# Kernel optimization log

Measured on AMD Instinct MI355X. Metric: run time of the kernel, lower is better.

Reference implementation:

```python
import jax, jax.numpy as jnp
import numpy as np

B, S, E = 2, 2048, 2048
H, G = 16, 4
HD = E // H          # 128
GD = HD * G          # 512
NGH = H // G         # 4 (tile factor for K/V heads)


def setup_inputs() -> dict:
    key = jax.random.key(0)
    ks = jax.random.split(key, 6)
    sc = 0.02
    return {
        "x": jax.random.normal(ks[0], (B, S, E), dtype=jnp.float32),
        "mask": jnp.ones((B, S, S), dtype=jnp.int32),
        "Wq": jax.random.normal(ks[1], (E, E), dtype=jnp.float32) * sc,
        "bq": jnp.zeros((E,), dtype=jnp.float32),
        "Wk": jax.random.normal(ks[2], (E, GD), dtype=jnp.float32) * sc,
        "bk": jnp.zeros((GD,), dtype=jnp.float32),
        "Wv": jax.random.normal(ks[3], (E, GD), dtype=jnp.float32) * sc,
        "bv": jnp.zeros((GD,), dtype=jnp.float32),
        "Wo": jax.random.normal(ks[4], (E, E), dtype=jnp.float32) * sc,
        "bo": jnp.zeros((E,), dtype=jnp.float32),
    }


def reference(x, mask, Wq, bq, Wk, bk, Wv, bv, Wo, bo):
    b, s, _ = x.shape
    # projections
    q = x @ Wq + bq                                   # [B,S,E]
    k = x @ Wk + bk                                   # [B,S,GD]
    v = x @ Wv + bv                                   # [B,S,GD]
    q = q.reshape(b, s, H, HD).transpose(0, 2, 1, 3)  # [B,H,S,hd]
    k = k.reshape(b, s, G, HD).transpose(0, 2, 1, 3)  # [B,G,S,hd]
    v = v.reshape(b, s, G, HD).transpose(0, 2, 1, 3)
    # torch .repeat(1, NGH, 1, 1): tile groups -> head h uses group h % G
    k = jnp.tile(k, (1, NGH, 1, 1))                   # [B,H,S,hd]
    v = jnp.tile(v, (1, NGH, 1, 1))
    scale = 1.0 / np.sqrt(HD).astype(np.float32)
    scores = jnp.einsum("bhqd,bhkd->bhqk", q, k) * scale
    m = mask[:, None, :, :]                           # [B,1,S,S]
    scores = jnp.where(m == 0, jnp.float32(-10000.0), scores)
    attn = jax.nn.softmax(scores, axis=-1)
    out = jnp.einsum("bhqk,bhkd->bhqd", attn, v)      # [B,H,S,hd]
    out = out.transpose(0, 2, 1, 3).reshape(b, s, E)  # [B,S,E]
    return out @ Wo + bo
```

## Files before the change

kernel.cpp:

```cpp
#include <hip/hip_runtime.h>

#define B_ 2
#define S_ 2048
#define E_ 2048
#define H_ 16
#define G_ 4
#define HD_ 128
#define GD_ 512
#define KVLD_ 1024
#define QKVN_ 3072
#define M_ (B_*S_)

using u16 = unsigned short;
using u32 = unsigned int;
typedef __attribute__((ext_vector_type(8))) short short8;
typedef __attribute__((ext_vector_type(4))) float f32x4;

#define QSCL 0.12751891114f
#define MASKED_L2 (-14427.0f)

__device__ __forceinline__ u16 f2bf(float f) {
  union { float f; unsigned u; } v; v.f = f;
  unsigned r = v.u + 0x7fff + ((v.u >> 16) & 1);
  return (u16)(r >> 16);
}

__device__ __forceinline__ void async16(const void* g, void* l) {
  __builtin_amdgcn_global_load_lds((const __attribute__((address_space(1))) unsigned int*)g,
                                   (__attribute__((address_space(3))) unsigned int*)l, 16, 0, 0);
}

__global__ __launch_bounds__(256) void cast_plus(const float* __restrict__ in,
                                                 u16* __restrict__ out, int n4,
                                                 const float* __restrict__ ba,
                                                 const float* __restrict__ bbk,
                                                 const float* __restrict__ bc,
                                                 float* __restrict__ bo) {
  if ((int)blockIdx.x >= (n4 + 255) / 256) {
    int t = (blockIdx.x - (n4 + 255) / 256) * 256 + threadIdx.x;
    if (t < 2048) bo[t] = ba[t];
    else if (t < 2560) bo[t] = bbk[t - 2048];
    else if (t < 3072) bo[t] = bc[t - 2560];
    return;
  }
  int i = blockIdx.x * 256 + threadIdx.x;
  if (i >= n4) return;
  float4 v = ((const float4*)in)[i];
  union { u16 o[4]; uint2 u; } pk;
  pk.o[0] = f2bf(v.x); pk.o[1] = f2bf(v.y); pk.o[2] = f2bf(v.z); pk.o[3] = f2bf(v.w);
  *(uint2*)(out + (size_t)i * 4) = pk.u;
}

__global__ __launch_bounds__(256) void transpose_cast4(const float* __restrict__ Wq,
                                                       const float* __restrict__ Wk,
                                                       const float* __restrict__ Wv,
                                                       const float* __restrict__ Wo,
                                                       u16* __restrict__ Wqkvt,
                                                       u16* __restrict__ Wot) {
  __shared__ u16 tile[64 * 72];
  int b = blockIdx.x;
  const float* W; u16* Wt; int N, bx;
  if (b < 1024)      { W = Wq; Wt = Wqkvt;                     N = E_;  bx = b;        }
  else if (b < 1280) { W = Wk; Wt = Wqkvt + (size_t)2048 * E_; N = GD_; bx = b - 1024; }
  else if (b < 1536) { W = Wv; Wt = Wqkvt + (size_t)2560 * E_; N = GD_; bx = b - 1280; }
  else               { W = Wo; Wt = Wot;                       N = E_;  bx = b - 1536; }
  int nbx = N / 64;
  int n0 = (bx % nbx) * 64, k0 = (bx / nbx) * 64;
  int t = threadIdx.x;
  int row = t >> 2;
  int seg = t & 3;
  const float* src = W + (size_t)(k0 + row) * N + n0 + seg * 16;
  #pragma unroll
  for (int i = 0; i < 4; ++i) {
    float4 v = *(const float4*)(src + i * 4);
    int nl = seg * 16 + i * 4;
    tile[(nl + 0) * 72 + row] = f2bf(v.x);
    tile[(nl + 1) * 72 + row] = f2bf(v.y);
    tile[(nl + 2) * 72 + row] = f2bf(v.z);
    tile[(nl + 3) * 72 + row] = f2bf(v.w);
  }
  __syncthreads();
  int nl = t >> 2, s2 = t & 3;
  u16* dst = Wt + (size_t)(n0 + nl) * E_ + k0 + s2 * 16;
  *(uint4*)dst       = *(const uint4*)&tile[nl * 72 + s2 * 16];
  *(uint4*)(dst + 8) = *(const uint4*)&tile[nl * 72 + s2 * 16 + 8];
}

__global__ __launch_bounds__(256) void transpose_v(const u16* __restrict__ KVb, u16* __restrict__ Vtg) {
  __shared__ u16 tile[64 * 72];
  int kv0 = blockIdx.x * 64;
  int gn0 = blockIdx.y * 64;
  int t = threadIdx.x;
  int row = t >> 2, seg = t & 3;
  int prow = (row & 15) * 4 + (row >> 4);
  const u16* src = KVb + (size_t)(kv0 + row) * KVLD_ + 512 + gn0 + seg * 16;
  union { uint4 v; u16 s[8]; } a, b;
  a.v = *(const uint4*)src; b.v = *(const uint4*)(src + 8);
  #pragma unroll
  for (int j = 0; j < 8; ++j) tile[(seg * 16 + j) * 72 + prow] = a.s[j];
  #pragma unroll
  for (int j = 0; j < 8; ++j) tile[(seg * 16 + 8 + j) * 72 + prow] = b.s[j];
  __syncthreads();
  int gl = t >> 2, ks2 = t & 3;
  int bb = kv0 >> 11;
  int s0 = kv0 & 2047;
  int gn = gn0 + gl;
  u16* dst = Vtg + (size_t)(bb * 512 + gn) * S_ + s0 + ks2 * 16;
  *(uint4*)dst       = *(const uint4*)&tile[gl * 72 + ks2 * 16];
  *(uint4*)(dst + 8) = *(const uint4*)&tile[gl * 72 + ks2 * 16 + 8];
}

__global__ __launch_bounds__(256) void mask_flags(const int* __restrict__ mask, int* __restrict__ flags) {
  int idx = blockIdx.x * 4 + (threadIdx.x >> 6);
  int lane = threadIdx.x & 63;
  int bb = idx >> 12, rg = (idx >> 5) & 127, kt = idx & 31;
  const int* base = mask + ((size_t)bb * S_ + rg * 16) * S_ + kt * 64;
  int row = lane >> 2, c0 = (lane & 3) * 16;
  int ok = 1;
  #pragma unroll
  for (int i = 0; i < 4; ++i) {
    int4 v = *(const int4*)&base[(size_t)row * S_ + c0 + i * 4];
    ok &= (v.x != 0) & (v.y != 0) & (v.z != 0) & (v.w != 0);
  }
  ok = __all(ok) ? 1 : 0;
  if (lane == 0) flags[idx] = ok;
}

__global__ __launch_bounds__(256) void gemm_qkv(const u16* __restrict__ A, const u16* __restrict__ Bt,
                                                const float* __restrict__ bias,
                                                u16* __restrict__ Qb, u16* __restrict__ KVb, int K) {
  __shared__ u16 As[2][128 * 32];
  __shared__ u16 Bs[2][128 * 32];
  int nbx = gridDim.x;
  int bid = blockIdx.y * nbx + blockIdx.x;
  int chunk = (nbx * gridDim.y) >> 3;
  int swz = (bid & 7) * chunk + (bid >> 3);
  int n0 = (swz % nbx) * 128, m0 = (swz / nbx) * 128;
  int t = threadIdx.x;
  int w = t >> 6, lane = t & 63, c = lane & 15, q = lane >> 4;
  int wm = w & 1, wn = w >> 1;
  int r0 = t >> 2;
  int kcs = ((t & 3) ^ ((t >> 3) & 3)) * 8;
  const u16* Ag0 = A  + (size_t)(m0 + r0) * K + kcs;
  const u16* Ag1 = A  + (size_t)(m0 + 64 + r0) * K + kcs;
  const u16* Bg0 = Bt + (size_t)(n0 + r0) * K + kcs;
  const u16* Bg1 = Bt + (size_t)(n0 + 64 + r0) * K + kcs;
  int roff = (q ^ ((c >> 1) & 3)) * 8;
  f32x4 acc[4][4] = {};
  async16(Ag0, &As[0][t * 8]);
  async16(Ag1, &As[0][2048 + t * 8]);
  async16(Bg0, &Bs[0][t * 8]);
  async16(Bg1, &Bs[0][2048 + t * 8]);
  for (int k0 = 0; k0 < K; k0 += 32) {
    int cur = (k0 >> 5) & 1;
    __syncthreads();
    if (k0 + 32 < K) {
      async16(Ag0 + k0 + 32, &As[cur ^ 1][t * 8]);
      async16(Ag1 + k0 + 32, &As[cur ^ 1][2048 + t * 8]);
      async16(Bg0 + k0 + 32, &Bs[cur ^ 1][t * 8]);
      async16(Bg1 + k0 + 32, &Bs[cur ^ 1][2048 + t * 8]);
    }
    short8 af[4], bf[4];
    #pragma unroll
    for (int i = 0; i < 4; ++i) {
      af[i] = *(const short8*)&As[cur][(wm * 64 + i * 16 + c) * 32 + roff];
      bf[i] = *(const short8*)&Bs[cur][(wn * 64 + i * 16 + c) * 32 + roff];
    }
    #pragma unroll
    for (int i = 0; i < 4; ++i)
      #pragma unroll
      for (int j = 0; j < 4; ++j)
        acc[i][j] = __builtin_amdgcn_mfma_f32_16x16x32_bf16(af[i], bf[j], acc[i][j], 0, 0, 0);
  }
  int isq = (n0 < 2048);
  #pragma unroll
  for (int i = 0; i < 4; ++i) {
    int mrow_base = m0 + wm * 64 + i * 16 + q * 4;
    #pragma unroll
    for (int j = 0; j < 4; ++j) {
      int coln = n0 + wn * 64 + j * 16 + c;
      float bv = bias[coln];
      #pragma unroll
      for (int r = 0; r < 4; ++r) {
        float v = acc[i][j][r] + bv;
        if (isq) Qb[(size_t)(mrow_base + r) * E_ + coln] = f2bf(v * QSCL);
        else     KVb[(size_t)(mrow_base + r) * KVLD_ + coln - 2048] = f2bf(v);
      }
    }
  }
}

__global__ __launch_bounds__(256) void gemm_k(const u16* __restrict__ A, const u16* __restrict__ Bt,
                                              const float* __restrict__ bias, float* __restrict__ Cout,
                                              int M, int N, int K) {
  __shared__ u16 As[2][128 * 32];
  __shared__ u16 Bs[2][128 * 32];
  int nbx = gridDim.x;
  int bid = blockIdx.y * nbx + blockIdx.x;
  int chunk = (nbx * gridDim.y) >> 3;
  int swz = (bid & 7) * chunk + (bid >> 3);
  int n0 = (swz % nbx) * 128, m0 = (swz / nbx) * 128;
  int t = threadIdx.x;
  int w = t >> 6, lane = t & 63, c = lane & 15, q = lane >> 4;
  int wm = w & 1, wn = w >> 1;
  int r0 = t >> 2;
  int kcs = ((t & 3) ^ ((t >> 3) & 3)) * 8;
  const u16* Ag0 = A  + (size_t)(m0 + r0) * K + kcs;
  const u16* Ag1 = A  + (size_t)(m0 + 64 + r0) * K + kcs;
  const u16* Bg0 = Bt + (size_t)(n0 + r0) * K + kcs;
  const u16* Bg1 = Bt + (size_t)(n0 + 64 + r0) * K + kcs;
  int roff = (q ^ ((c >> 1) & 3)) * 8;
  f32x4 acc[4][4] = {};
  async16(Ag0, &As[0][t * 8]);
  async16(Ag1, &As[0][2048 + t * 8]);
  async16(Bg0, &Bs[0][t * 8]);
  async16(Bg1, &Bs[0][2048 + t * 8]);
  for (int k0 = 0; k0 < K; k0 += 32) {
    int cur = (k0 >> 5) & 1;
    __syncthreads();
    if (k0 + 32 < K) {
      async16(Ag0 + k0 + 32, &As[cur ^ 1][t * 8]);
      async16(Ag1 + k0 + 32, &As[cur ^ 1][2048 + t * 8]);
      async16(Bg0 + k0 + 32, &Bs[cur ^ 1][t * 8]);
      async16(Bg1 + k0 + 32, &Bs[cur ^ 1][2048 + t * 8]);
    }
    short8 af[4], bf[4];
    #pragma unroll
    for (int i = 0; i < 4; ++i) {
      af[i] = *(const short8*)&As[cur][(wm * 64 + i * 16 + c) * 32 + roff];
      bf[i] = *(const short8*)&Bs[cur][(wn * 64 + i * 16 + c) * 32 + roff];
    }
    #pragma unroll
    for (int i = 0; i < 4; ++i)
      #pragma unroll
      for (int j = 0; j < 4; ++j)
        acc[i][j] = __builtin_amdgcn_mfma_f32_16x16x32_bf16(af[i], bf[j], acc[i][j], 0, 0, 0);
  }
  #pragma unroll
  for (int i = 0; i < 4; ++i) {
    int mrow_base = m0 + wm * 64 + i * 16 + q * 4;
    #pragma unroll
    for (int j = 0; j < 4; ++j) {
      int coln = n0 + wn * 64 + j * 16 + c;
      float bv = bias[coln];
      #pragma unroll
      for (int r = 0; r < 4; ++r)
        Cout[(size_t)(mrow_base + r) * N + coln] = acc[i][j][r] + bv;
    }
  }
}

__global__ __launch_bounds__(512) void attn_k(const u16* __restrict__ Q, const u16* __restrict__ KVb,
                                              const u16* __restrict__ Vtg, const int* __restrict__ mask,
                                              const int* __restrict__ mflags, u16* __restrict__ O) {
  __shared__ u16 Ks[2][64 * 128];
  __shared__ u16 Vs[2][128 * 64];
  __shared__ u16 Ps[8 * 16 * 64];
  int bid = blockIdx.x;
  int mt = bid & 15, h = (bid >> 4) & 15, bb = bid >> 8;
  int g = h & 3;
  int t = threadIdx.x, w = t >> 6, lane = t & 63, c = lane & 15, q = lane >> 4;
  int m0 = mt * 128;

  const u16* Qbase  = Q   + (size_t)(bb * S_ + m0) * E_ + h * HD_;
  const u16* Kbase  = KVb + (size_t)bb * S_ * KVLD_ + g * HD_;
  const u16* Vtbase = Vtg + (size_t)(bb * G_ + g) * HD_ * S_;

  int krow0 = t >> 4;
  int kkc   = ((t & 15) ^ (krow0 & 15)) * 8;
  const u16* Kst = Kbase + (size_t)krow0 * KVLD_ + kkc;
  int vn0 = t >> 3;
  int vkc = ((t & 7) ^ (vn0 & 7)) * 8;
  const u16* Vst = Vtbase + (size_t)vn0 * S_ + vkc;

  int pwa[4], pra[2];
  #pragma unroll
  for (int r = 0; r < 4; ++r) {
    int row = q * 4 + r;
    pwa[r] = w * 1024 + row * 64 + (((c >> 1) ^ (row & 7)) * 8) + (c & 1) * 4;
  }
  #pragma unroll
  for (int ks = 0; ks < 2; ++ks)
    pra[ks] = w * 1024 + c * 64 + (((ks * 4 + q) ^ (c & 7)) * 8);

  short8 aq[4];
  #pragma unroll
  for (int k0 = 0; k0 < 4; ++k0)
    aq[k0] = *(const short8*)&Qbase[(size_t)(w * 16 + c) * E_ + k0 * 32 + q * 8];

  const short8 ones = {(short)0x3F80, (short)0x3F80, (short)0x3F80, (short)0x3F80,
                       (short)0x3F80, (short)0x3F80, (short)0x3F80, (short)0x3F80};

  f32x4 Oa[8] = {};
  f32x4 lacc = {};

  #pragma unroll
  for (int p = 0; p < 2; ++p)
    async16(Kst + (size_t)(p * 32) * KVLD_, &Ks[0][p * 4096 + t * 8]);
  #pragma unroll
  for (int p = 0; p < 2; ++p)
    async16(Vst + (size_t)(p * 64) * S_, &Vs[0][p * 4096 + t * 8]);

  for (int kv0 = 0; kv0 < S_; kv0 += 64) {
    int cur = (kv0 >> 6) & 1;
    __syncthreads();
    if (kv0 + 64 < S_) {
      #pragma unroll
      for (int p = 0; p < 2; ++p)
        async16(Kst + (size_t)(kv0 + 64 + p * 32) * KVLD_, &Ks[cur ^ 1][p * 4096 + t * 8]);
      #pragma unroll
      for (int p = 0; p < 2; ++p)
        async16(Vst + (size_t)(p * 64) * S_ + kv0 + 64, &Vs[cur ^ 1][p * 4096 + t * 8]);
    }
    const u16* K_ = Ks[cur];
    const u16* V_ = Vs[cur];

    f32x4 sc[4] = {};
    #pragma unroll
    for (int k0 = 0; k0 < 4; ++k0) {
      short8 bk[4];
      #pragma unroll
      for (int ns = 0; ns < 4; ++ns)
        bk[ns] = *(const short8*)&K_[(ns * 16 + c) * 128 + (((k0 * 4 + q) ^ c) * 8)];
      #pragma unroll
      for (int ns = 0; ns < 4; ++ns)
        sc[ns] = __builtin_amdgcn_mfma_f32_16x16x32_bf16(aq[k0], bk[ns], sc[ns], 0, 0, 0);
    }
    {
      int flag = mflags[bb * 4096 + (mt * 8 + w) * 32 + (kv0 >> 6)];
      if (!flag) {
        #pragma unroll
        for (int r = 0; r < 4; ++r) {
          int qrow = m0 + w * 16 + q * 4 + r;
          const int* mrow = mask + ((size_t)bb * S_ + qrow) * S_ + kv0;
          #pragma unroll
          for (int ns = 0; ns < 4; ++ns)
            if (mrow[ns * 16 + c] == 0) sc[ns][r] = MASKED_L2;
        }
      }
    }
    #pragma unroll
    for (int r = 0; r < 4; ++r) {
      u32 u[4];
      #pragma unroll
      for (int ns = 0; ns < 4; ++ns) {
        float p = __builtin_amdgcn_exp2f(sc[ns][r]);
        u[ns] = __float_as_uint(p) + 0x8000u;
      }
      uint2 pk;
      pk.x = __builtin_amdgcn_perm(u[1], u[0], 0x07060302);
      pk.y = __builtin_amdgcn_perm(u[3], u[2], 0x07060302);
      *(uint2*)&Ps[pwa[r]] = pk;
    }
    __asm__ volatile("" ::: "memory");
    #pragma unroll
    for (int ks = 0; ks < 2; ++ks) {
      short8 ap = *(const short8*)&Ps[pra[ks]];
      lacc = __builtin_amdgcn_mfma_f32_16x16x32_bf16(ap, ones, lacc, 0, 0, 0);
      #pragma unroll
      for (int d = 0; d < 8; ++d) {
        short8 bv = *(const short8*)&V_[(d * 16 + c) * 64 + (((ks * 4 + q) ^ (c & 7)) * 8)];
        Oa[d] = __builtin_amdgcn_mfma_f32_16x16x32_bf16(ap, bv, Oa[d], 0, 0, 0);
      }
    }
  }
  {
    float inv[4];
    #pragma unroll
    for (int r = 0; r < 4; ++r) inv[r] = 1.0f / lacc[r];
    #pragma unroll
    for (int d = 0; d < 8; ++d)
      #pragma unroll
      for (int r = 0; r < 4; ++r) {
        size_t off = (size_t)(bb * S_ + m0 + w * 16 + q * 4 + r) * E_ + h * HD_ + d * 16 + c;
        O[off] = f2bf(Oa[d][r] * inv[r]);
      }
  }
}

extern "C" void kernel_launch(void* const* d_in, const int* in_sizes, int n_in,
                              void* d_out, int out_size, void* d_ws, size_t ws_size,
                              hipStream_t stream) {
  const float* x    = (const float*)d_in[0];
  const int*   mask = (const int*)d_in[1];
  const float* Wq   = (const float*)d_in[2];
  const float* bq   = (const float*)d_in[3];
  const float* Wk   = (const float*)d_in[4];
  const float* bk   = (const float*)d_in[5];
  const float* Wv   = (const float*)d_in[6];
  const float* bv   = (const float*)d_in[7];
  const float* Wo   = (const float*)d_in[8];
  const float* bo   = (const float*)d_in[9];
  float* out = (float*)d_out;

  char* ws = (char*)d_ws;
  u16* xb    = (u16*)ws; ws += (size_t)M_ * E_ * 2;
  u16* Wqkvt = (u16*)ws; ws += (size_t)QKVN_ * E_ * 2;
  u16* Wot   = (u16*)ws; ws += (size_t)E_ * E_ * 2;
  u16* Qb    = (u16*)ws; ws += (size_t)M_ * E_ * 2;
  u16* KVb   = (u16*)ws; ws += (size_t)M_ * KVLD_ * 2;
  u16* Ob    = (u16*)ws; ws += (size_t)M_ * E_ * 2;
  u16* Vtg   = (u16*)ws; ws += (size_t)B_ * G_ * HD_ * S_ * 2;
  int* mfl   = (int*)ws; ws += (size_t)B_ * 128 * 32 * 4;
  float* bqkv = (float*)ws; ws += QKVN_ * 4;

  int n4 = M_ * E_ / 4;
  cast_plus<<<(n4 + 255) / 256 + 12, 256, 0, stream>>>(x, xb, n4, bq, bk, bv, bqkv);
  transpose_cast4<<<2560, 256, 0, stream>>>(Wq, Wk, Wv, Wo, Wqkvt, Wot);
  mask_flags<<<B_ * 128 * 32 / 4, 256, 0, stream>>>(mask, mfl);

  gemm_qkv<<<dim3(QKVN_ / 128, M_ / 128), 256, 0, stream>>>(xb, Wqkvt, bqkv, Qb, KVb, E_);
  transpose_v<<<dim3(M_ / 64, GD_ / 64), 256, 0, stream>>>(KVb, Vtg);

  attn_k<<<B_ * H_ * (S_ / 128), 512, 0, stream>>>(Qb, KVb, Vtg, mask, mfl, Ob);

  gemm_k<<<dim3(E_ / 128, M_ / 128), 256, 0, stream>>>(Ob, Wot, bo, out, M_, E_, E_);
}
```

Measured before the change: 343.2 us.

## Restructure attention to 4 waves each owning 32 query rows with 32-key tiles

The attention kernel drops from 8 waves to 4 per block, and each wave now handles two 16-row query slices. This lets each loaded K and V fragment feed two MFMAs, halving LDS reads per MFMA. The KV tile shrinks from 64 to 32 keys, so LDS buffers shrink and the P-tile and V-transpose permutation layouts change to match. The cost is more loop iterations and barriers, fewer waves for latency hiding, and a mask-flag lookup indexed at 64-key granularity that is now read twice per 64 keys.

```diff
diff --git a/kernel.cpp b/kernel.cpp
--- a/kernel.cpp
+++ b/kernel.cpp
@@ -92,7 +92,8 @@
   int gn0 = blockIdx.y * 64;
   int t = threadIdx.x;
   int row = t >> 2, seg = t & 3;
-  int prow = (row & 15) * 4 + (row >> 4);
+  int r32 = row & 31;
+  int prow = (row & 32) + (r32 & 15) * 2 + (r32 >> 4);
   const u16* src = KVb + (size_t)(kv0 + row) * KVLD_ + 512 + gn0 + seg * 16;
   union { uint4 v; u16 s[8]; } a, b;
   a.v = *(const uint4*)src; b.v = *(const uint4*)(src + 8);
@@ -250,12 +251,12 @@
   }
 }
 
-__global__ __launch_bounds__(512) void attn_k(const u16* __restrict__ Q, const u16* __restrict__ KVb,
+__global__ __launch_bounds__(256) void attn_k(const u16* __restrict__ Q, const u16* __restrict__ KVb,
                                               const u16* __restrict__ Vtg, const int* __restrict__ mask,
                                               const int* __restrict__ mflags, u16* __restrict__ O) {
-  __shared__ u16 Ks[2][64 * 128];
-  __shared__ u16 Vs[2][128 * 64];
-  __shared__ u16 Ps[8 * 16 * 64];
+  __shared__ u16 Ks[2][32 * 128];
+  __shared__ u16 Vs[2][128 * 32];
+  __shared__ u16 Ps[8 * 16 * 32];
   int bid = blockIdx.x;
   int mt = bid & 15, h = (bid >> 4) & 15, bb = bid >> 8;
   int g = h & 3;
@@ -267,113 +268,113 @@
   const u16* Vtbase = Vtg + (size_t)(bb * G_ + g) * HD_ * S_;
 
   int krow0 = t >> 4;
-  int kkc   = ((t & 15) ^ (krow0 & 15)) * 8;
+  int kkc   = ((t & 15) ^ krow0) * 8;
   const u16* Kst = Kbase + (size_t)krow0 * KVLD_ + kkc;
-  int vn0 = t >> 3;
-  int vkc = ((t & 7) ^ (vn0 & 7)) * 8;
+  int vn0 = t >> 2;
+  int vkc = ((t & 3) ^ ((t >> 3) & 3)) * 8;
   const u16* Vst = Vtbase + (size_t)vn0 * S_ + vkc;
 
-  int pwa[4], pra[2];
-  #pragma unroll
-  for (int r = 0; r < 4; ++r) {
-    int row = q * 4 + r;
-    pwa[r] = w * 1024 + row * 64 + (((c >> 1) ^ (row & 7)) * 8) + (c & 1) * 4;
-  }
-  #pragma unroll
-  for (int ks = 0; ks < 2; ++ks)
-    pra[ks] = w * 1024 + c * 64 + (((ks * 4 + q) ^ (c & 7)) * 8);
-
-  short8 aq[4];
-  #pragma unroll
-  for (int k0 = 0; k0 < 4; ++k0)
-    aq[k0] = *(const short8*)&Qbase[(size_t)(w * 16 + c) * E_ + k0 * 32 + q * 8];
+  int pwa[2][4], pra[2];
+  #pragma unroll
+  for (int s = 0; s < 2; ++s) {
+    #pragma unroll
+    for (int r = 0; r < 4; ++r) {
+      int row = q * 4 + r;
+      pwa[s][r] = (w * 2 + s) * 512 + row * 32 + (((c >> 2) ^ ((row >> 1) & 3)) << 3) + ((c & 3) << 1);
+    }
+    pra[s] = (w * 2 + s) * 512 + c * 32 + ((q ^ ((c >> 1) & 3)) << 3);
+  }
+
+  short8 aq[2][4];
+  #pragma unroll
+  for (int s = 0; s < 2; ++s)
+    #pragma unroll
+    for (int k0 = 0; k0 < 4; ++k0)
+      aq[s][k0] = *(const short8*)&Qbase[(size_t)(w * 32 + s * 16 + c) * E_ + k0 * 32 + q * 8];
 
   const short8 ones = {(short)0x3F80, (short)0x3F80, (short)0x3F80, (short)0x3F80,
                        (short)0x3F80, (short)0x3F80, (short)0x3F80, (short)0x3F80};
 
-  f32x4 Oa[8] = {};
-  f32x4 lacc = {};
+  f32x4 Oa[2][8] = {};
+  f32x4 lacc[2] = {};
 
   #pragma unroll
   for (int p = 0; p < 2; ++p)
-    async16(Kst + (size_t)(p * 32) * KVLD_, &Ks[0][p * 4096 + t * 8]);
+    async16(Kst + (size_t)(p * 16) * KVLD_, &Ks[0][p * 2048 + t * 8]);
   #pragma unroll
   for (int p = 0; p < 2; ++p)
-    async16(Vst + (size_t)(p * 64) * S_, &Vs[0][p * 4096 + t * 8]);
-
-  for (int kv0 = 0; kv0 < S_; kv0 += 64) {
-    int cur = (kv0 >> 6) & 1;
+    async16(Vst + (size_t)(p * 64) * S_, &Vs[0][p * 2048 + t * 8]);
+
+  for (int kv0 = 0; kv0 < S_; kv0 += 32) {
+    int cur = (kv0 >> 5) & 1;
     __syncthreads();
-    if (kv0 + 64 < S_) {
+    if (kv0 + 32 < S_) {
       #pragma unroll
       for (int p = 0; p < 2; ++p)
-        async16(Kst + (size_t)(kv0 + 64 + p * 32) * KVLD_, &Ks[cur ^ 1][p * 4096 + t * 8]);
+        async16(Kst + (size_t)(kv0 + 32 + p * 16) * KVLD_, &Ks[cur ^ 1][p * 2048 + t * 8]);
       #pragma unroll
       for (int p = 0; p < 2; ++p)
-        async16(Vst + (size_t)(p * 64) * S_ + kv0 + 64, &Vs[cur ^ 1][p * 4096 + t * 8]);
+        async16(Vst + (size_t)(p * 64) * S_ + kv0 + 32, &Vs[cur ^ 1][p * 2048 + t * 8]);
     }
     const u16* K_ = Ks[cur];
     const u16* V_ = Vs[cur];
 
-    f32x4 sc[4] = {};
+    f32x4 sc[2][2] = {};
     #pragma unroll
     for (int k0 = 0; k0 < 4; ++k0) {
-      short8 bk[4];
-      #pragma unroll
-      for (int ns = 0; ns < 4; ++ns)
-        bk[ns] = *(const short8*)&K_[(ns * 16 + c) * 128 + (((k0 * 4 + q) ^ c) * 8)];
-      #pragma unroll
-      for (int ns = 0; ns < 4; ++ns)
-        sc[ns] = __builtin_amdgcn_mfma_f32_16x16x32_bf16(aq[k0], bk[ns], sc[ns], 0, 0, 0);
-    }
-    {
-      int flag = mflags[bb * 4096 + (mt * 8 + w) * 32 + (kv0 >> 6)];
+      int koff = (((k0 * 4 + q) ^ c) * 8);
+      short8 bk0 = *(const short8*)&K_[c * 128 + koff];
+      short8 bk1 = *(const short8*)&K_[(16 + c) * 128 + koff];
+      #pragma unroll
+      for (int s = 0; s < 2; ++s) {
+        sc[s][0] = __builtin_amdgcn_mfma_f32_16x16x32_bf16(aq[s][k0], bk0, sc[s][0], 0, 0, 0);
+        sc[s][1] = __builtin_amdgcn_mfma_f32_16x16x32_bf16(aq[s][k0], bk1, sc[s][1], 0, 0, 0);
+      }
+    }
+    #pragma unroll
+    for (int s = 0; s < 2; ++s) {
+      int flag = mflags[bb * 4096 + (mt * 8 + w * 2 + s) * 32 + (kv0 >> 6)];
       if (!flag) {
         #pragma unroll
         for (int r = 0; r < 4; ++r) {
-          int qrow = m0 + w * 16 + q * 4 + r;
+          int qrow = m0 + w * 32 + s * 16 + q * 4 + r;
           const int* mrow = mask + ((size_t)bb * S_ + qrow) * S_ + kv0;
-          #pragma unroll
-          for (int ns = 0; ns < 4; ++ns)
-            if (mrow[ns * 16 + c] == 0) sc[ns][r] = MASKED_L2;
+          if (mrow[c] == 0)      sc[s][0][r] = MASKED_L2;
+          if (mrow[16 + c] == 0) sc[s][1][r] = MASKED_L2;
         }
       }
     }
     #pragma unroll
-    for (int r = 0; r < 4; ++r) {
-      u32 u[4];
-      #pragma unroll
-      for (int ns = 0; ns < 4; ++ns) {
-        float p = __builtin_amdgcn_exp2f(sc[ns][r]);
-        u[ns] = __float_as_uint(p) + 0x8000u;
+    for (int s = 0; s < 2; ++s)
+      #pragma unroll
+      for (int r = 0; r < 4; ++r) {
+        u32 u0 = __float_as_uint(__builtin_amdgcn_exp2f(sc[s][0][r])) + 0x8000u;
+        u32 u1 = __float_as_uint(__builtin_amdgcn_exp2f(sc[s][1][r])) + 0x8000u;
+        *(u32*)&Ps[pwa[s][r]] = __builtin_amdgcn_perm(u1, u0, 0x07060302);
       }
-      uint2 pk;
-      pk.x = __builtin_amdgcn_perm(u[1], u[0], 0x07060302);
-      pk.y = __builtin_amdgcn_perm(u[3], u[2], 0x07060302);
-      *(uint2*)&Ps[pwa[r]] = pk;
-    }
     __asm__ volatile("" ::: "memory");
-    #pragma unroll
-    for (int ks = 0; ks < 2; ++ks) {
-      short8 ap = *(const short8*)&Ps[pra[ks]];
-      lacc = __builtin_amdgcn_mfma_f32_16x16x32_bf16(ap, ones, lacc, 0, 0, 0);
-      #pragma unroll
-      for (int d = 0; d < 8; ++d) {
-        short8 bv = *(const short8*)&V_[(d * 16 + c) * 64 + (((ks * 4 + q) ^ (c & 7)) * 8)];
-        Oa[d] = __builtin_amdgcn_mfma_f32_16x16x32_bf16(ap, bv, Oa[d], 0, 0, 0);
-      }
-    }
-  }
-  {
+    short8 ap0 = *(const short8*)&Ps[pra[0]];
+    short8 ap1 = *(const short8*)&Ps[pra[1]];
+    lacc[0] = __builtin_amdgcn_mfma_f32_16x16x32_bf16(ap0, ones, lacc[0], 0, 0, 0);
+    lacc[1] = __builtin_amdgcn_mfma_f32_16x16x32_bf16(ap1, ones, lacc[1], 0, 0, 0);
+    #pragma unroll
+    for (int d = 0; d < 8; ++d) {
+      short8 bv = *(const short8*)&V_[(d * 16 + c) * 32 + ((q ^ ((c >> 1) & 3)) * 8)];
+      Oa[0][d] = __builtin_amdgcn_mfma_f32_16x16x32_bf16(ap0, bv, Oa[0][d], 0, 0, 0);
+      Oa[1][d] = __builtin_amdgcn_mfma_f32_16x16x32_bf16(ap1, bv, Oa[1][d], 0, 0, 0);
+    }
+  }
+  #pragma unroll
+  for (int s = 0; s < 2; ++s) {
     float inv[4];
     #pragma unroll
-    for (int r = 0; r < 4; ++r) inv[r] = 1.0f / lacc[r];
+    for (int r = 0; r < 4; ++r) inv[r] = 1.0f / lacc[s][r];
     #pragma unroll
     for (int d = 0; d < 8; ++d)
       #pragma unroll
       for (int r = 0; r < 4; ++r) {
-        size_t off = (size_t)(bb * S_ + m0 + w * 16 + q * 4 + r) * E_ + h * HD_ + d * 16 + c;
-        O[off] = f2bf(Oa[d][r] * inv[r]);
+        size_t off = (size_t)(bb * S_ + m0 + w * 32 + s * 16 + q * 4 + r) * E_ + h * HD_ + d * 16 + c;
+        O[off] = f2bf(Oa[s][d][r] * inv[r]);
       }
   }
 }
@@ -412,7 +413,7 @@
   gemm_qkv<<<dim3(QKVN_ / 128, M_ / 128), 256, 0, stream>>>(xb, Wqkvt, bqkv, Qb, KVb, E_);
   transpose_v<<<dim3(M_ / 64, GD_ / 64), 256, 0, stream>>>(KVb, Vtg);
 
-  attn_k<<<B_ * H_ * (S_ / 128), 512, 0, stream>>>(Qb, KVb, Vtg, mask, mfl, Ob);
+  attn_k<<<B_ * H_ * (S_ / 128), 256, 0, stream>>>(Qb, KVb, Vtg, mask, mfl, Ob);
 
   gemm_k<<<dim3(E_ / 128, M_ / 128), 256, 0, stream>>>(Ob, Wot, bo, out, M_, E_, E_);
 }
```

After: 355.9 us. 3.7% more time.
